# Performance work log

Hardware: AMD Instinct MI355X
Metric: run time of the kernel (lower is better)

Reference implementation:

```python
import jax, jax.numpy as jnp
import numpy as np

B, S, H = 2, 2048, 2048
NH, G = 16, 4
HD = H // NH          # 128
REP = NH // G         # 4 query heads per KV group
KV = G * HD           # 512


def setup_inputs() -> dict:
    key = jax.random.key(0)
    ks = jax.random.split(key, 10)
    s = 0.02
    X = jax.random.normal(ks[0], (B, S, H), dtype=jnp.float32)
    Wq = jax.random.normal(ks[1], (H, H), dtype=jnp.float32) * s
    bq = jnp.zeros((H,), dtype=jnp.float32)
    Wk = jax.random.normal(ks[2], (H, KV), dtype=jnp.float32) * s
    bk = jnp.zeros((KV,), dtype=jnp.float32)
    Wv = jax.random.normal(ks[3], (H, KV), dtype=jnp.float32) * s
    bv = jnp.zeros((KV,), dtype=jnp.float32)
    Wo = jax.random.normal(ks[4], (H, H), dtype=jnp.float32) * s
    bo = jnp.zeros((H,), dtype=jnp.float32)
    # causal mask: 1 where attention is disallowed (strict upper triangle)
    casual_mask = jnp.triu(jnp.ones((S, S), dtype=jnp.float32), k=1)[None, None]
    return {"X": X, "Wq": Wq, "bq": bq, "Wk": Wk, "bk": bk,
            "Wv": Wv, "bv": bv, "Wo": Wo, "bo": bo,
            "casual_mask": casual_mask}


def reference(X, Wq, bq, Wk, bk, Wv, bv, Wo, bo, casual_mask):
    # projections
    q = X @ Wq + bq                          # [B,S,H]
    k = X @ Wk + bk                          # [B,S,G*HD]
    v = X @ Wv + bv                          # [B,S,G*HD]
    # split heads; q grouped as (group, rep) to match torch expand ordering
    q = q.reshape(B, S, NH, HD).transpose(0, 2, 1, 3)       # [B,NH,S,HD]
    q = q.reshape(B, G, REP, S, HD)                          # [B,G,REP,S,HD]
    k = k.reshape(B, S, G, HD).transpose(0, 2, 1, 3)         # [B,G,S,HD]
    v = v.reshape(B, S, G, HD).transpose(0, 2, 1, 3)         # [B,G,S,HD]
    scale = 1.0 / jnp.sqrt(jnp.float32(HD))
    scores = jnp.einsum('bgrqd,bgkd->bgrqk', q, k) * scale   # [B,G,REP,S,S]
    scores = scores + casual_mask * (-1e9)
    probs = jax.nn.softmax(scores, axis=-1)
    out = jnp.einsum('bgrqk,bgkd->bgrqd', probs, v)          # [B,G,REP,S,HD]
    out = out.reshape(B, NH, S, HD).transpose(0, 2, 1, 3).reshape(B, S, H)
    return out @ Wo + bo
```

## Files before the change

kernel.cpp:

```cpp
#include <hip/hip_runtime.h>

#define B_   2
#define S_   2048
#define H_   2048
#define NH_  16
#define G_   4
#define HD_  128
#define KV_  512
#define HQKV 3072

typedef __attribute__((ext_vector_type(8))) short bf16x8;
typedef __attribute__((ext_vector_type(4))) float f32x4;

__device__ __forceinline__ unsigned short f2bf(float f) {
    unsigned u = __float_as_uint(f);
    u += 0x7fff + ((u >> 16) & 1);
    return (unsigned short)(u >> 16);
}

__global__ void k_cvt_bf16(const float* __restrict__ in, unsigned short* __restrict__ out, int n4) {
    int i = blockIdx.x * blockDim.x + threadIdx.x;
    if (i >= n4) return;
    float4 v = ((const float4*)in)[i];
    ushort4 o;
    o.x = f2bf(v.x); o.y = f2bf(v.y); o.z = f2bf(v.z); o.w = f2bf(v.w);
    ((ushort4*)out)[i] = o;
}

__global__ void k_transpose_cvt(const float* __restrict__ in, unsigned short* __restrict__ out,
                                int R, int C) {
    __shared__ float t[32][33];
    int c0 = blockIdx.x * 32, r0 = blockIdx.y * 32;
    int tx = threadIdx.x, ty = threadIdx.y;
#pragma unroll
    for (int i = 0; i < 4; ++i)
        t[ty + i*8][tx] = in[(size_t)(r0 + ty + i*8) * C + c0 + tx];
    __syncthreads();
#pragma unroll
    for (int i = 0; i < 4; ++i)
        out[(size_t)(c0 + ty + i*8) * R + r0 + tx] = f2bf(t[tx][ty + i*8]);
}

__global__ void k_concat_bias(const float* __restrict__ bq, const float* __restrict__ bk,
                              const float* __restrict__ bv, float* __restrict__ out) {
    int i = blockIdx.x * 256 + threadIdx.x;
    if (i >= HQKV) return;
    out[i] = (i < H_) ? bq[i] : (i < H_ + KV_ ? bk[i - H_] : bv[i - H_ - KV_]);
}

__global__ void k_transpose_v(const unsigned short* __restrict__ in, unsigned short* __restrict__ out) {
    __shared__ unsigned short t[32][33];
    int b = blockIdx.z;
    int c0 = blockIdx.x * 32, s0 = blockIdx.y * 32;
    int tx = threadIdx.x, ty = threadIdx.y;
#pragma unroll
    for (int i = 0; i < 4; ++i)
        t[ty + i*8][tx] = in[((size_t)b * S_ + s0 + ty + i*8) * HQKV + (H_ + KV_) + c0 + tx];
    __syncthreads();
#pragma unroll
    for (int i = 0; i < 4; ++i)
        out[((size_t)b * KV_ + c0 + ty + i*8) * S_ + s0 + tx] = t[tx][ty + i*8];
}

#define GLDS16(gsrc, ldst)                                                            \
    __builtin_amdgcn_global_load_lds(                                                 \
        (const __attribute__((address_space(1))) void*)(gsrc),                        \
        (__attribute__((address_space(3))) void*)(ldst), 16, 0, 0)

template <bool BF16OUT>
__global__ __launch_bounds__(256) void k_gemm_bt(
    const unsigned short* __restrict__ A, const unsigned short* __restrict__ Bt,
    const float* __restrict__ bias, void* __restrict__ Cout, int M, int N, int K) {
    __shared__ __align__(16) unsigned short As[128 * 64];
    __shared__ __align__(16) unsigned short Bs[128 * 64];
    const int tid = threadIdx.x, lane = tid & 63, w = tid >> 6;
    const int l15 = lane & 15, l4 = lane >> 4;
    const int wr = w >> 1, wc = w & 1;
    const int m0 = blockIdx.x * 128, n0 = blockIdx.y * 128;
    f32x4 acc[4][4] = {};

    for (int kt = 0; kt < K; kt += 64) {
        __syncthreads();
#pragma unroll
        for (int i = 0; i < 4; ++i) {
            int p = (w * 4 + i) * 64 + lane;
            int row = p >> 3, c = (p & 7) ^ (row & 7);
            GLDS16(A + (size_t)(m0 + row) * K + kt + c * 8, As + (size_t)(w * 4 + i) * 512);
        }
#pragma unroll
        for (int i = 0; i < 4; ++i) {
            int p = (w * 4 + i) * 64 + lane;
            int row = p >> 3, c = (p & 7) ^ (row & 7);
            GLDS16(Bt + (size_t)(n0 + row) * K + kt + c * 8, Bs + (size_t)(w * 4 + i) * 512);
        }
        __syncthreads();
#pragma unroll
        for (int ks = 0; ks < 2; ++ks) {
            bf16x8 af[4], bfr[4];
#pragma unroll
            for (int m = 0; m < 4; ++m) {
                int row = wr * 64 + m * 16 + l15;
                int ch = (ks * 4 + l4) ^ (row & 7);
                af[m] = *(const bf16x8*)(As + row * 64 + ch * 8);
            }
#pragma unroll
            for (int n = 0; n < 4; ++n) {
                int row = wc * 64 + n * 16 + l15;
                int ch = (ks * 4 + l4) ^ (row & 7);
                bfr[n] = *(const bf16x8*)(Bs + row * 64 + ch * 8);
            }
#pragma unroll
            for (int m = 0; m < 4; ++m)
#pragma unroll
                for (int n = 0; n < 4; ++n)
                    acc[m][n] = __builtin_amdgcn_mfma_f32_16x16x32_bf16(af[m], bfr[n], acc[m][n], 0, 0, 0);
        }
    }
#pragma unroll
    for (int m = 0; m < 4; ++m) {
        int row = m0 + wr * 64 + m * 16 + l4 * 4;
#pragma unroll
        for (int n = 0; n < 4; ++n) {
            int col = n0 + wc * 64 + n * 16 + l15;
            float bv = bias[col];
#pragma unroll
            for (int r = 0; r < 4; ++r) {
                float v = acc[m][n][r] + bv;
                if (BF16OUT)
                    ((unsigned short*)Cout)[(size_t)(row + r) * N + col] = f2bf(v);
                else
                    ((float*)Cout)[(size_t)(row + r) * N + col] = v;
            }
        }
    }
}

__global__ __launch_bounds__(256) void k_flash(
    const unsigned short* __restrict__ QKV,
    const unsigned short* __restrict__ VT,
    unsigned short* __restrict__ Oa) {
    __shared__ __align__(16) unsigned short Ks[64][132];
    __shared__ __align__(16) unsigned short Vs[128][68];
    __shared__ __align__(16) unsigned short Ps[4][16][68];
    const int tid = threadIdx.x, lane = tid & 63, w = tid >> 6;
    const int l15 = lane & 15, l4 = lane >> 4;
    const int pr = blockIdx.x;
    const int bh = blockIdx.y;
    const int b = bh >> 4, nh = bh & 15, g = nh >> 2;
    const float sc2 = 0.08838834764831843f * 1.4426950408889634f;

    for (int half = 0; half < 2; ++half) {
        const int qt = half ? (31 - pr) : pr;
        const int q0 = qt * 64;
        const int qbase = q0 + w * 16;

        bf16x8 qf[4];
#pragma unroll
        for (int kb = 0; kb < 4; ++kb)
            qf[kb] = *(const bf16x8*)(QKV + (size_t)(b * S_ + qbase + l15) * HQKV +
                                      nh * HD_ + kb * 32 + l4 * 8);

        f32x4 o[8] = {};
        float mrow[4], lrow[4];
#pragma unroll
        for (int r = 0; r < 4; ++r) { mrow[r] = -1e30f; lrow[r] = 0.f; }

        const int nkt = qt + 1;
        for (int kt = 0; kt < nkt; ++kt) {
            const int kv0 = kt * 64;
            __syncthreads();
#pragma unroll
            for (int i = 0; i < 4; ++i) {
                int f = i * 256 + tid;
                int row = f >> 4, c = f & 15;
                *(bf16x8*)(&Ks[row][c * 8]) =
                    *(const bf16x8*)(QKV + (size_t)(b * S_ + kv0 + row) * HQKV + H_ + g * HD_ + c * 8);
            }
#pragma unroll
            for (int i = 0; i < 4; ++i) {
                int f = i * 256 + tid;
                int row = f >> 3, c = f & 7;
                *(bf16x8*)(&Vs[row][c * 8]) =
                    *(const bf16x8*)(VT + ((size_t)b * KV_ + g * HD_ + row) * S_ + kv0 + c * 8);
            }
            __syncthreads();

            f32x4 s[4] = {};
#pragma unroll
            for (int kb = 0; kb < 4; ++kb) {
                bf16x8 kf[4];
#pragma unroll
                for (int n = 0; n < 4; ++n)
                    kf[n] = *(const bf16x8*)(&Ks[n * 16 + l15][kb * 32 + l4 * 8]);
#pragma unroll
                for (int n = 0; n < 4; ++n)
                    s[n] = __builtin_amdgcn_mfma_f32_16x16x32_bf16(qf[kb], kf[n], s[n], 0, 0, 0);
            }
            if (kv0 + 63 > qbase) {
#pragma unroll
                for (int n = 0; n < 4; ++n)
#pragma unroll
                    for (int r = 0; r < 4; ++r) {
                        int kcol = kv0 + n * 16 + l15;
                        int qrow = qbase + l4 * 4 + r;
                        s[n][r] = (kcol <= qrow) ? s[n][r] * sc2 : -1e30f;
                    }
            } else {
#pragma unroll
                for (int n = 0; n < 4; ++n)
#pragma unroll
                    for (int r = 0; r < 4; ++r) s[n][r] *= sc2;
            }
            float sf[4];
#pragma unroll
            for (int r = 0; r < 4; ++r) {
                float vm = fmaxf(fmaxf(s[0][r], s[1][r]), fmaxf(s[2][r], s[3][r]));
                vm = fmaxf(vm, __shfl_xor(vm, 1));
                vm = fmaxf(vm, __shfl_xor(vm, 2));
                vm = fmaxf(vm, __shfl_xor(vm, 4));
                vm = fmaxf(vm, __shfl_xor(vm, 8));
                float mn = fmaxf(mrow[r], vm);
                sf[r] = exp2f(mrow[r] - mn);
                mrow[r] = mn;
            }
            float rs[4] = {0.f, 0.f, 0.f, 0.f};
#pragma unroll
            for (int n = 0; n < 4; ++n)
#pragma unroll
                for (int r = 0; r < 4; ++r) {
                    float p = exp2f(s[n][r] - mrow[r]);
                    s[n][r] = p;
                    rs[r] += p;
                }
#pragma unroll
            for (int r = 0; r < 4; ++r) {
                float t = rs[r];
                t += __shfl_xor(t, 1); t += __shfl_xor(t, 2);
                t += __shfl_xor(t, 4); t += __shfl_xor(t, 8);
                lrow[r] = lrow[r] * sf[r] + t;
            }
#pragma unroll
            for (int nc = 0; nc < 8; ++nc) {
                f32x4 t = o[nc];
                t[0] *= sf[0]; t[1] *= sf[1]; t[2] *= sf[2]; t[3] *= sf[3];
                o[nc] = t;
            }
#pragma unroll
            for (int n = 0; n < 4; ++n)
#pragma unroll
                for (int r = 0; r < 4; ++r)
                    Ps[w][l4 * 4 + r][n * 16 + l15] = f2bf(s[n][r]);
#pragma unroll
            for (int kb = 0; kb < 2; ++kb) {
                bf16x8 pf = *(const bf16x8*)(&Ps[w][l15][kb * 32 + l4 * 8]);
#pragma unroll
                for (int nc = 0; nc < 8; ++nc) {
                    bf16x8 vf = *(const bf16x8*)(&Vs[nc * 16 + l15][kb * 32 + l4 * 8]);
                    o[nc] = __builtin_amdgcn_mfma_f32_16x16x32_bf16(pf, vf, o[nc], 0, 0, 0);
                }
            }
        }
#pragma unroll
        for (int r = 0; r < 4; ++r) {
            float inv = 1.0f / lrow[r];
            int qrow = qbase + l4 * 4 + r;
            size_t base = (size_t)(b * S_ + qrow) * H_ + nh * HD_;
#pragma unroll
            for (int nc = 0; nc < 8; ++nc)
                Oa[base + nc * 16 + l15] = f2bf(o[nc][r] * inv);
        }
    }
}

extern "C" void kernel_launch(void* const* d_in, const int* in_sizes, int n_in,
                              void* d_out, int out_size, void* d_ws, size_t ws_size,
                              hipStream_t stream) {
    const float* X  = (const float*)d_in[0];
    const float* Wq = (const float*)d_in[1];
    const float* bq = (const float*)d_in[2];
    const float* Wk = (const float*)d_in[3];
    const float* bk = (const float*)d_in[4];
    const float* Wv = (const float*)d_in[5];
    const float* bv = (const float*)d_in[6];
    const float* Wo = (const float*)d_in[7];
    const float* bo = (const float*)d_in[8];
    float* out = (float*)d_out;

    if (ws_size < 67200000) return;
    char* ws = (char*)d_ws;
    unsigned short* Xb   = (unsigned short*)(ws);
    unsigned short* WqkvT= (unsigned short*)(ws + 16777216);
    unsigned short* WoT  = (unsigned short*)(ws + 29360128);
    unsigned short* QKV  = (unsigned short*)(ws + 37748736);
    unsigned short* VbT  = (unsigned short*)(ws + 62914560);
    float*          bqkv = (float*)(ws + 67108864);
    unsigned short* AOb  = Xb;

    k_cvt_bf16<<<(B_ * S_ * H_ / 4 + 255) / 256, 256, 0, stream>>>(X, Xb, B_ * S_ * H_ / 4);
    k_transpose_cvt<<<dim3(H_ / 32, H_ / 32), dim3(32, 8), 0, stream>>>(Wq, WqkvT, H_, H_);
    k_transpose_cvt<<<dim3(KV_ / 32, H_ / 32), dim3(32, 8), 0, stream>>>(Wk, WqkvT + (size_t)H_ * H_, H_, KV_);
    k_transpose_cvt<<<dim3(KV_ / 32, H_ / 32), dim3(32, 8), 0, stream>>>(Wv, WqkvT + (size_t)(H_ + KV_) * H_, H_, KV_);
    k_transpose_cvt<<<dim3(H_ / 32, H_ / 32), dim3(32, 8), 0, stream>>>(Wo, WoT, H_, H_);
    k_concat_bias<<<(HQKV + 255) / 256, 256, 0, stream>>>(bq, bk, bv, bqkv);

    k_gemm_bt<true><<<dim3(32, 24), 256, 0, stream>>>(Xb, WqkvT, bqkv, QKV, 4096, HQKV, 2048);

    k_transpose_v<<<dim3(KV_ / 32, S_ / 32, B_), dim3(32, 8), 0, stream>>>(QKV, VbT);
    k_flash<<<dim3(16, 32), 256, 0, stream>>>(QKV, VbT, AOb);

    k_gemm_bt<false><<<dim3(32, 16), 256, 0, stream>>>(AOb, WoT, bo, out, 4096, 2048, 2048);
}
```

Baseline: 257.6 us.

## Double-buffer flash attention K/V via direct-to-LDS loads with swizzle and lazy rescale

The flash kernel now loads K and V tiles straight into LDS with global_load_lds into two buffers, prefetching the next tile while computing the current one, and XOR-swizzles the LDS layout in place of padding. The softmax scale is folded into Q at load time, and the running max plus output rescale are skipped unless some row's max grows by more than 8 (log2 units). Blocks are remapped over a 1D grid so heads sharing KV data land on the same XCD, aiming for better L2 reuse. The goal is to hide global load latency and cut per-tile ALU work, at the cost of more LDS use and a small extra rounding error from pre-scaling Q in bf16.

```diff
diff --git a/kernel.cpp b/kernel.cpp
--- a/kernel.cpp
+++ b/kernel.cpp
@@ -17,6 +17,14 @@
     u += 0x7fff + ((u >> 16) & 1);
     return (unsigned short)(u >> 16);
 }
+__device__ __forceinline__ float bf2f(unsigned short s) {
+    return __uint_as_float(((unsigned)s) << 16);
+}
+
+#define GLDS16(gsrc, ldst)                                                            \
+    __builtin_amdgcn_global_load_lds(                                                 \
+        (const __attribute__((address_space(1))) void*)(gsrc),                        \
+        (__attribute__((address_space(3))) void*)(ldst), 16, 0, 0)
 
 __global__ void k_cvt_bf16(const float* __restrict__ in, unsigned short* __restrict__ out, int n4) {
     int i = blockIdx.x * blockDim.x + threadIdx.x;
@@ -61,11 +69,6 @@
     for (int i = 0; i < 4; ++i)
         out[((size_t)b * KV_ + c0 + ty + i*8) * S_ + s0 + tx] = t[tx][ty + i*8];
 }
-
-#define GLDS16(gsrc, ldst)                                                            \
-    __builtin_amdgcn_global_load_lds(                                                 \
-        (const __attribute__((address_space(1))) void*)(gsrc),                        \
-        (__attribute__((address_space(3))) void*)(ldst), 16, 0, 0)
 
 template <bool BF16OUT>
 __global__ __launch_bounds__(256) void k_gemm_bt(
@@ -139,15 +142,20 @@
     const unsigned short* __restrict__ QKV,
     const unsigned short* __restrict__ VT,
     unsigned short* __restrict__ Oa) {
-    __shared__ __align__(16) unsigned short Ks[64][132];
-    __shared__ __align__(16) unsigned short Vs[128][68];
+    __shared__ __align__(16) unsigned short Ks[2][64 * 128];
+    __shared__ __align__(16) unsigned short Vs[2][128 * 64];
     __shared__ __align__(16) unsigned short Ps[4][16][68];
     const int tid = threadIdx.x, lane = tid & 63, w = tid >> 6;
     const int l15 = lane & 15, l4 = lane >> 4;
-    const int pr = blockIdx.x;
-    const int bh = blockIdx.y;
+    const int bid = blockIdx.x;
+    const int xcd = bid & 7, idx = bid >> 3;
+    const int bh = xcd * 4 + (idx & 3);
+    const int pr = idx >> 2;
     const int b = bh >> 4, nh = bh & 15, g = nh >> 2;
     const float sc2 = 0.08838834764831843f * 1.4426950408889634f;
+
+    const unsigned short* kgbase = QKV + (size_t)b * S_ * HQKV + H_ + g * HD_;
+    const unsigned short* vgbase = VT + ((size_t)b * KV_ + g * HD_) * S_;
 
     for (int half = 0; half < 2; ++half) {
         const int qt = half ? (31 - pr) : pr;
@@ -156,42 +164,51 @@
 
         bf16x8 qf[4];
 #pragma unroll
-        for (int kb = 0; kb < 4; ++kb)
-            qf[kb] = *(const bf16x8*)(QKV + (size_t)(b * S_ + qbase + l15) * HQKV +
-                                      nh * HD_ + kb * 32 + l4 * 8);
+        for (int kb = 0; kb < 4; ++kb) {
+            bf16x8 raw = *(const bf16x8*)(QKV + (size_t)(b * S_ + qbase + l15) * HQKV +
+                                          nh * HD_ + kb * 32 + l4 * 8);
+            bf16x8 sq;
+#pragma unroll
+            for (int e = 0; e < 8; ++e)
+                sq[e] = (short)f2bf(bf2f((unsigned short)raw[e]) * sc2);
+            qf[kb] = sq;
+        }
 
         f32x4 o[8] = {};
         float mrow[4], lrow[4];
 #pragma unroll
         for (int r = 0; r < 4; ++r) { mrow[r] = -1e30f; lrow[r] = 0.f; }
 
-        const int nkt = qt + 1;
-        for (int kt = 0; kt < nkt; ++kt) {
+        auto issue = [&](int kt, int cb) {
             const int kv0 = kt * 64;
-            __syncthreads();
 #pragma unroll
             for (int i = 0; i < 4; ++i) {
-                int f = i * 256 + tid;
-                int row = f >> 4, c = f & 15;
-                *(bf16x8*)(&Ks[row][c * 8]) =
-                    *(const bf16x8*)(QKV + (size_t)(b * S_ + kv0 + row) * HQKV + H_ + g * HD_ + c * 8);
+                int p = i * 256 + tid;
+                int row = p >> 4, c = (p & 15) ^ (row & 15);
+                GLDS16(kgbase + (size_t)(kv0 + row) * HQKV + c * 8,
+                       &Ks[cb][(i * 256 + w * 64) * 8]);
             }
 #pragma unroll
             for (int i = 0; i < 4; ++i) {
-                int f = i * 256 + tid;
-                int row = f >> 3, c = f & 7;
-                *(bf16x8*)(&Vs[row][c * 8]) =
-                    *(const bf16x8*)(VT + ((size_t)b * KV_ + g * HD_ + row) * S_ + kv0 + c * 8);
-            }
-            __syncthreads();
-
+                int p = i * 256 + tid;
+                int row = p >> 3, c = (p & 7) ^ (row & 7);
+                GLDS16(vgbase + (size_t)row * S_ + kv0 + c * 8,
+                       &Vs[cb][(i * 256 + w * 64) * 8]);
+            }
+        };
+
+        auto compute = [&](int cb, int kt) {
+            const int kv0 = kt * 64;
             f32x4 s[4] = {};
 #pragma unroll
             for (int kb = 0; kb < 4; ++kb) {
                 bf16x8 kf[4];
 #pragma unroll
-                for (int n = 0; n < 4; ++n)
-                    kf[n] = *(const bf16x8*)(&Ks[n * 16 + l15][kb * 32 + l4 * 8]);
+                for (int n = 0; n < 4; ++n) {
+                    int row = n * 16 + l15;
+                    int sl = (kb * 4 + l4) ^ (row & 15);
+                    kf[n] = *(const bf16x8*)(&Ks[cb][(row * 16 + sl) * 8]);
+                }
 #pragma unroll
                 for (int n = 0; n < 4; ++n)
                     s[n] = __builtin_amdgcn_mfma_f32_16x16x32_bf16(qf[kb], kf[n], s[n], 0, 0, 0);
@@ -203,25 +220,37 @@
                     for (int r = 0; r < 4; ++r) {
                         int kcol = kv0 + n * 16 + l15;
                         int qrow = qbase + l4 * 4 + r;
-                        s[n][r] = (kcol <= qrow) ? s[n][r] * sc2 : -1e30f;
+                        if (kcol > qrow) s[n][r] = -1e30f;
                     }
-            } else {
-#pragma unroll
-                for (int n = 0; n < 4; ++n)
-#pragma unroll
-                    for (int r = 0; r < 4; ++r) s[n][r] *= sc2;
-            }
-            float sf[4];
+            }
+            float vm[4];
 #pragma unroll
             for (int r = 0; r < 4; ++r) {
-                float vm = fmaxf(fmaxf(s[0][r], s[1][r]), fmaxf(s[2][r], s[3][r]));
-                vm = fmaxf(vm, __shfl_xor(vm, 1));
-                vm = fmaxf(vm, __shfl_xor(vm, 2));
-                vm = fmaxf(vm, __shfl_xor(vm, 4));
-                vm = fmaxf(vm, __shfl_xor(vm, 8));
-                float mn = fmaxf(mrow[r], vm);
-                sf[r] = exp2f(mrow[r] - mn);
-                mrow[r] = mn;
+                float v = fmaxf(fmaxf(s[0][r], s[1][r]), fmaxf(s[2][r], s[3][r]));
+                v = fmaxf(v, __shfl_xor(v, 1));
+                v = fmaxf(v, __shfl_xor(v, 2));
+                v = fmaxf(v, __shfl_xor(v, 4));
+                v = fmaxf(v, __shfl_xor(v, 8));
+                vm[r] = v;
+            }
+            int needs = 0;
+#pragma unroll
+            for (int r = 0; r < 4; ++r) needs |= (vm[r] > mrow[r] + 8.0f) ? 1 : 0;
+            if (__any(needs)) {
+                float sf[4];
+#pragma unroll
+                for (int r = 0; r < 4; ++r) {
+                    float mn = fmaxf(mrow[r], vm[r]);
+                    sf[r] = exp2f(mrow[r] - mn);
+                    mrow[r] = mn;
+                    lrow[r] *= sf[r];
+                }
+#pragma unroll
+                for (int nc = 0; nc < 8; ++nc) {
+                    f32x4 t = o[nc];
+                    t[0] *= sf[0]; t[1] *= sf[1]; t[2] *= sf[2]; t[3] *= sf[3];
+                    o[nc] = t;
+                }
             }
             float rs[4] = {0.f, 0.f, 0.f, 0.f};
 #pragma unroll
@@ -237,13 +266,7 @@
                 float t = rs[r];
                 t += __shfl_xor(t, 1); t += __shfl_xor(t, 2);
                 t += __shfl_xor(t, 4); t += __shfl_xor(t, 8);
-                lrow[r] = lrow[r] * sf[r] + t;
-            }
-#pragma unroll
-            for (int nc = 0; nc < 8; ++nc) {
-                f32x4 t = o[nc];
-                t[0] *= sf[0]; t[1] *= sf[1]; t[2] *= sf[2]; t[3] *= sf[3];
-                o[nc] = t;
+                lrow[r] += t;
             }
 #pragma unroll
             for (int n = 0; n < 4; ++n)
@@ -255,11 +278,30 @@
                 bf16x8 pf = *(const bf16x8*)(&Ps[w][l15][kb * 32 + l4 * 8]);
 #pragma unroll
                 for (int nc = 0; nc < 8; ++nc) {
-                    bf16x8 vf = *(const bf16x8*)(&Vs[nc * 16 + l15][kb * 32 + l4 * 8]);
+                    int row = nc * 16 + l15;
+                    int sl = (kb * 4 + l4) ^ (row & 7);
+                    bf16x8 vf = *(const bf16x8*)(&Vs[cb][(row * 8 + sl) * 8]);
                     o[nc] = __builtin_amdgcn_mfma_f32_16x16x32_bf16(pf, vf, o[nc], 0, 0, 0);
                 }
             }
-        }
+        };
+
+        const int nkt = qt + 1;
+        __syncthreads();
+        issue(0, 0);
+        asm volatile("s_waitcnt vmcnt(0)" ::: "memory");
+        __builtin_amdgcn_s_barrier();
+        __builtin_amdgcn_sched_barrier(0);
+
+        for (int kt = 0; kt < nkt; ++kt) {
+            const int cb = kt & 1;
+            if (kt + 1 < nkt) issue(kt + 1, cb ^ 1);
+            compute(cb, kt);
+            asm volatile("s_waitcnt vmcnt(0) lgkmcnt(0)" ::: "memory");
+            __builtin_amdgcn_s_barrier();
+            __builtin_amdgcn_sched_barrier(0);
+        }
+
 #pragma unroll
         for (int r = 0; r < 4; ++r) {
             float inv = 1.0f / lrow[r];
@@ -306,7 +348,7 @@
     k_gemm_bt<true><<<dim3(32, 24), 256, 0, stream>>>(Xb, WqkvT, bqkv, QKV, 4096, HQKV, 2048);
 
     k_transpose_v<<<dim3(KV_ / 32, S_ / 32, B_), dim3(32, 8), 0, stream>>>(QKV, VbT);
-    k_flash<<<dim3(16, 32), 256, 0, stream>>>(QKV, VbT, AOb);
+    k_flash<<<dim3(512), 256, 0, stream>>>(QKV, VbT, AOb);
 
     k_gemm_bt<false><<<dim3(32, 16), 256, 0, stream>>>(AOb, WoT, bo, out, 4096, 2048, 2048);
 }
```

New measurement: 240.3 us. 6.7% less time.
